# Kernel optimization log

Measured on AMD Instinct MI355X. Metric: run time of the kernel, lower is better.

## Reference

```python
import jax, jax.numpy as jnp
import numpy as np

B, S, I = 4096, 128, 8
H = 512
L = 3


def setup_inputs() -> dict:
    key = jax.random.key(0)
    ks = jax.random.split(key, 5)
    scale = 1.0 / np.sqrt(H)
    return {
        "input": jax.random.normal(ks[0], (B, S, I), dtype=jnp.float32),
        "Wih": jax.random.normal(ks[1], (L, 3 * H, I), dtype=jnp.float32) * scale,
        "Whh": jax.random.normal(ks[2], (L, 3 * H, H), dtype=jnp.float32) * scale,
        "bih": jax.random.normal(ks[3], (L, 3 * H), dtype=jnp.float32) * scale,
        "bhh": jax.random.normal(ks[4], (L, 3 * H), dtype=jnp.float32) * scale,
    }


def _gru_cell(x, h, Wih, Whh, bih, bhh):
    # PyTorch GRUCell gate order: reset, update, new
    gi = x @ Wih.T + bih            # [B, 3H]
    gh = h @ Whh.T + bhh            # [B, 3H]
    i_r, i_z, i_n = jnp.split(gi, 3, axis=-1)
    h_r, h_z, h_n = jnp.split(gh, 3, axis=-1)
    r = jax.nn.sigmoid(i_r + h_r)
    z = jax.nn.sigmoid(i_z + h_z)
    n = jnp.tanh(i_n + r * h_n)
    return (1.0 - z) * n + z * h


def reference(input, Wih, Whh, bih, bhh):
    batch = input.shape[0]
    h0 = jnp.zeros((batch, Wih.shape[1] // 3), dtype=input.dtype)

    def step(h, x_t):
        # each layer consumes the same raw input x_t, chaining the context
        for l in range(Wih.shape[0]):
            h = _gru_cell(x_t, h, Wih[l], Whh[l], bih[l], bhh[l])
        return h, None

    xs = jnp.swapaxes(input, 0, 1)  # [S, B, I]
    h_final, _ = jax.lax.scan(step, h0, xs)
    return h_final
```

## Files before the change

### kernel.cpp

```cpp
#include <hip/hip_runtime.h>

typedef __attribute__((ext_vector_type(8))) short short8;
typedef __attribute__((ext_vector_type(4))) float f32x4;
typedef __attribute__((ext_vector_type(4))) int   i32x4;

#define MFMA(a,b,c)  __builtin_amdgcn_mfma_f32_16x16x32_bf16(a,b,c,0,0,0)
#define MFMAI(a,b,c) __builtin_amdgcn_mfma_i32_16x16x64_i8(a,b,c,0,0,0)

#define S_LEN 128
#define IN_D  8
#define HID   512
#define NL    3
#define H8STR 528
#define LOG2E  1.4426950408889634f
#define LOG2E2 2.8853901617779268f
#define WKL_STRIDE ((size_t)(32 * 8 * 3 * 64 * 16))

#define OFF_WI8  0
#define OFF_WIH  (2359296)
#define OFF_SW   (2359296 + 294912)
#define OFF_SWI  (OFF_SW + 18432)
#define OFF_FLAG (OFF_SWI + 18432)
#define OFF_XCHG (OFF_FLAG + 1024)

__device__ __forceinline__ unsigned short f2bf(float f){
  unsigned u = __float_as_uint(f);
  u += 0x7FFFu + ((u >> 16) & 1u);
  return (unsigned short)(u >> 16);
}
__device__ __forceinline__ float fexp2(float x){ return __builtin_amdgcn_exp2f(x); }
__device__ __forceinline__ float frcp(float x){ return __builtin_amdgcn_rcpf(x); }

__global__ void prep_scale(const float* __restrict__ Whh,
                           float* __restrict__ sw, float* __restrict__ swi){
  int row = blockIdx.x * 4 + (threadIdx.x >> 6);
  int lane = threadIdx.x & 63;
  const float* src = Whh + (size_t)row * 512;
  float m = 0.f;
#pragma unroll
  for (int i = 0; i < 8; ++i) m = fmaxf(m, fabsf(src[lane + i * 64]));
#pragma unroll
  for (int off = 32; off; off >>= 1) m = fmaxf(m, (float)__shfl_xor(m, off));
  m = fmaxf(m, 1e-20f);
  if (lane == 0){ sw[row] = m / 127.f; swi[row] = 127.f / m; }
}

__global__ void prep_wi8(const float* __restrict__ Whh, const float* __restrict__ swi,
                         unsigned char* __restrict__ Wp8){
  int gid = blockIdx.x * 256 + threadIdx.x;
  int lane = gid & 63;
  int r = gid >> 6;
  int g  = r % 3;  r /= 3;
  int kk = r & 7;  r >>= 3;
  int nt = r & 31;
  int l  = r >> 5;
  int row = l * 1536 + g * 512 + nt * 16 + (lane & 15);
  int k0  = kk * 64 + (lane >> 4) * 16;
  const float* src = Whh + (size_t)row * 512 + k0;
  float si = swi[row];
  uint4 v = {0,0,0,0};
  unsigned w[4] = {0,0,0,0};
#pragma unroll
  for (int j = 0; j < 16; ++j){
    int q = (int)rintf(src[j] * si);
    q = q > 127 ? 127 : (q < -127 ? -127 : q);
    w[j >> 2] |= ((unsigned)(q & 0xFF)) << ((j & 3) * 8);
  }
  v.x = w[0]; v.y = w[1]; v.z = w[2]; v.w = w[3];
  *(uint4*)(Wp8 + (size_t)gid * 16) = v;
}

__global__ void prep_wih(const float* __restrict__ Wih, unsigned short* __restrict__ Wip){
  int gid = blockIdx.x * 256 + threadIdx.x;
  int lane = gid & 63;
  int r = gid >> 6;
  int g  = r % 3;  r /= 3;
  int nt = r & 31;
  int l  = r >> 5;
  float scl = (g == 2) ? LOG2E2 : LOG2E;
  unsigned short t[8] = {0,0,0,0,0,0,0,0};
  if ((lane >> 4) == 0){
    int n = g * 512 + nt * 16 + (lane & 15);
    const float* src = Wih + ((size_t)l * 1536 + n) * 8;
#pragma unroll
    for (int j = 0; j < 8; ++j) t[j] = f2bf(src[j] * scl);
  }
  uint4 v;
  v.x = t[0] | ((unsigned)t[1] << 16);
  v.y = t[2] | ((unsigned)t[3] << 16);
  v.z = t[4] | ((unsigned)t[5] << 16);
  v.w = t[6] | ((unsigned)t[7] << 16);
  *(uint4*)(Wip + (size_t)gid * 8) = v;
}

__global__ __launch_bounds__(1024) void gru_main(
    const float* __restrict__ x,
    const unsigned char* __restrict__ Wp8,
    const unsigned short* __restrict__ Wip,
    const float* __restrict__ bih,
    const float* __restrict__ bhh,
    const float* __restrict__ sw,
    float* __restrict__ out,
    int* __restrict__ flags,
    unsigned int* __restrict__ xchg)
{
  __shared__ __align__(16) unsigned char  hB8[2][32 * H8STR];
  __shared__ __align__(16) unsigned short xpack[2][1024];
  __shared__ __align__(16) float sBrz[3 * 1024];
  __shared__ __align__(16) float sBni[3 * 512];
  __shared__ __align__(16) float sBnh[3 * 512];
  __shared__ __align__(16) float sK[4608];
  __shared__ int   pad[1024];

  const int tid  = threadIdx.x;
  const int wv   = tid >> 6;
  const int lane = tid & 63;
  const int l15  = lane & 15;
  const int l4   = lane >> 4;

  const int bid     = blockIdx.x;
  const int bgroup  = ((bid >> 3) << 2) | (bid & 3);
  const int half    = (bid >> 2) & 1;
  const int partner = bid ^ 4;
  const int b0      = bgroup * 32;
  const int lc      = wv * 16 + l4 * 4;
  const int colv    = half * 256 + lc;
  const int ntc     = half * 16 + wv;
  const int pcb0    = (1 - half) * 256;
  const int ko0     = half * 4;
  const int pk0     = 4 - ko0;

  if (flags[bid] == -1) pad[tid] = tid;

  unsigned int* xown = xchg + (size_t)bid * 4096;
  const unsigned int* xpb = xchg + (size_t)partner * 4096 + tid;
  const int dOff = (tid >> 6) * H8STR + pcb0 + (tid & 63) * 4;

  for (int i = tid; i < 2 * 32 * H8STR / 4; i += 1024) ((unsigned*)hB8)[i] = 0;
  for (int i = tid; i < 3072; i += 1024){
    int l = i >> 10, c = i & 1023;
    sBrz[i] = (bih[l * 1536 + c] + bhh[l * 1536 + c]) * LOG2E;
  }
  for (int i = tid; i < 1536; i += 1024){
    int l = i >> 9, c = i & 511;
    sBni[i] = bih[l * 1536 + 1024 + c] * LOG2E2;
    sBnh[i] = bhh[l * 1536 + 1024 + c] * LOG2E2;
  }
  for (int i = tid; i < 4608; i += 1024){
    int g = (i % 1536) >> 9;
    sK[i] = sw[i] * (1.f / 127.f) * (g == 2 ? LOG2E2 : LOG2E);
  }

  float hreg[2][4];
#pragma unroll
  for (int nf = 0; nf < 2; ++nf)
#pragma unroll
    for (int qq = 0; qq < 4; ++qq) hreg[nf][qq] = 0.f;

  const int xl = (tid >> 3) & 63;
  const size_t xbase = ((size_t)(b0 + (tid >> 9) * 16 + (xl & 15))) * (S_LEN * IN_D) + (tid & 7);
  const int xvalid = (xl < 16);
  { float xv = xvalid ? x[xbase] : 0.f; xpack[0][tid] = f2bf(xv); }
  __syncthreads();

  const int boff0 = l15 * H8STR + l4 * 16;
  const int boff1 = boff0 + 16 * H8STR;

  const unsigned char*  wklB = Wp8 + (size_t)ntc * (8 * 3 * 64 * 16) + (size_t)lane * 16;
  const unsigned short* wilB = Wip + (size_t)ntc * 3 * 512 + (size_t)lane * 8;

#define KSEQ(i) ((i) < 4 ? (ko0 + (i)) : (pk0 + (i) - 4))
#define WLD(S, i, P) { const unsigned char* w_ = (P) + KSEQ(i) * 3072; \
    wR##S = *(const i32x4*)(w_); \
    wZ##S = *(const i32x4*)(w_ + 1024); \
    wN##S = *(const i32x4*)(w_ + 2048); }
#define CONS(S, i) { \
    i32x4 hb0 = *(const i32x4*)(hb8c + boff0 + KSEQ(i) * 64); \
    i32x4 hb1 = *(const i32x4*)(hb8c + boff1 + KSEQ(i) * 64); \
    aR[0] = MFMAI(wR##S, hb0, aR[0]);  aR[1] = MFMAI(wR##S, hb1, aR[1]); \
    aZ[0] = MFMAI(wZ##S, hb0, aZ[0]);  aZ[1] = MFMAI(wZ##S, hb1, aZ[1]); \
    aN[0] = MFMAI(wN##S, hb0, aN[0]);  aN[1] = MFMAI(wN##S, hb1, aN[1]); }

  i32x4 wRa, wZa, wNa, wRb, wZb, wNb;
  WLD(a, 0, wklB)  WLD(b, 1, wklB)

  int cur = 0;
#pragma unroll 1
  for (int t = 0; t < S_LEN; ++t){
    const unsigned short* xp = &xpack[t & 1][0];
#pragma unroll 1
    for (int l = 0; l < NL; ++l){
      const int s    = t * NL + l;
      const int last = (s == S_LEN * NL - 1);
      const unsigned char* hb8c = hB8[cur];
      unsigned char*       hb8w = hB8[cur];
      unsigned char*       hb8n = hB8[cur ^ 1];
      const unsigned char*  wkl = wklB + (size_t)l * WKL_STRIDE;
      const unsigned short* wil = wilB + (size_t)l * (32 * 3 * 512);

      unsigned c0 = 0, c1 = 0;
      if (s > 0){
        while (__hip_atomic_load(&flags[partner], __ATOMIC_RELAXED, __HIP_MEMORY_SCOPE_AGENT) < s)
          __builtin_amdgcn_s_sleep(4);
        const unsigned int* src = xpb + ((s - 1) & 1) * 2048;
        c0 = __hip_atomic_load(src,        __ATOMIC_RELAXED, __HIP_MEMORY_SCOPE_AGENT);
        c1 = __hip_atomic_load(src + 1024, __ATOMIC_RELAXED, __HIP_MEMORY_SCOPE_AGENT);
      }

      i32x4 aR[2], aZ[2], aN[2];
#pragma unroll
      for (int nf = 0; nf < 2; ++nf){
        aR[nf] = (i32x4){0,0,0,0};
        aZ[nf] = (i32x4){0,0,0,0};
        aN[nf] = (i32x4){0,0,0,0};
      }

      CONS(a, 0)  WLD(a, 2, wkl)
      CONS(b, 1)  WLD(b, 3, wkl)
      CONS(a, 2)  WLD(a, 4, wkl)
      CONS(b, 3)  WLD(b, 5, wkl)

      if (s > 0){
        *(unsigned*)(hb8w + dOff)              = c0;
        *(unsigned*)(hb8w + dOff + 16 * H8STR) = c1;
      }
      asm volatile("s_waitcnt lgkmcnt(0)" ::: "memory");
      __builtin_amdgcn_s_barrier();

      short8 wiR = *(const short8*)(wil);
      short8 wiZ = *(const short8*)(wil + 512);
      short8 wiN = *(const short8*)(wil + 1024);

      CONS(a, 4)  WLD(a, 6, wkl)
      CONS(b, 5)  WLD(b, 7, wkl)
      CONS(a, 6)
      CONS(b, 7)

      {
        const unsigned char* wkn = wklB + (size_t)(l == NL - 1 ? 0 : l + 1) * WKL_STRIDE;
        WLD(a, 0, wkn)  WLD(b, 1, wkn)
      }

      const f32x4 vR4  = *(const f32x4*)&sBrz[l * 1024 + colv];
      const f32x4 vZ4  = *(const f32x4*)&sBrz[l * 1024 + 512 + colv];
      const f32x4 vNi4 = *(const f32x4*)&sBni[l * 512 + colv];
      const f32x4 vNh4 = *(const f32x4*)&sBnh[l * 512 + colv];
      const f32x4 kR4  = *(const f32x4*)&sK[l * 1536 + colv];
      const f32x4 kZ4  = *(const f32x4*)&sK[l * 1536 + 512 + colv];
      const f32x4 kN4  = *(const f32x4*)&sK[l * 1536 + 1024 + colv];

      f32x4 gR[2], gZ[2], gN[2];
      gR[0] = vR4;  gR[1] = vR4;
      gZ[0] = vZ4;  gZ[1] = vZ4;
      gN[0] = vNi4; gN[1] = vNi4;
      {
        short8 xb0 = *(const short8*)(xp + lane * 8);
        short8 xb1 = *(const short8*)(xp + 512 + lane * 8);
        gR[0] = MFMA(wiR, xb0, gR[0]);  gR[1] = MFMA(wiR, xb1, gR[1]);
        gZ[0] = MFMA(wiZ, xb0, gZ[0]);  gZ[1] = MFMA(wiZ, xb1, gZ[1]);
        gN[0] = MFMA(wiN, xb0, gN[0]);  gN[1] = MFMA(wiN, xb1, gN[1]);
      }

      unsigned int* xob = xown + (s & 1) * 2048;
#pragma unroll
      for (int nf = 0; nf < 2; ++nf){
        unsigned pk = 0;
#pragma unroll
        for (int qq = 0; qq < 4; ++qq){
          float rp = gR[nf][qq] + (float)aR[nf][qq] * kR4[qq];
          float zp = gZ[nf][qq] + (float)aZ[nf][qq] * kZ4[qq];
          float r  = frcp(1.f + fexp2(-rp));
          float z  = frcp(1.f + fexp2(-zp));
          float an = gN[nf][qq] + r * ((float)aN[nf][qq] * kN4[qq] + vNh4[qq]);
          float n  = fmaf(-2.f, frcp(1.f + fexp2(an)), 1.f);
          float hn = fmaf(z, hreg[nf][qq] - n, n);
          hreg[nf][qq] = hn;
          int hq = (int)rintf(hn * 127.f);
          pk |= ((unsigned)(hq & 0xFF)) << (qq * 8);
        }
        int brow = nf * 16 + l15;
        *(unsigned*)(hb8n + brow * H8STR + colv) = pk;
        if (!last)
          __hip_atomic_store(xob + brow * 64 + wv * 4 + l4, pk,
                             __ATOMIC_RELAXED, __HIP_MEMORY_SCOPE_AGENT);
      }

      if (l == NL - 1 && t < S_LEN - 1){
        float xv = xvalid ? x[xbase + (size_t)(t + 1) * IN_D] : 0.f;
        xpack[(t + 1) & 1][tid] = f2bf(xv);
      }

      if (!last){
        asm volatile("s_waitcnt vmcnt(0)" ::: "memory");
        __syncthreads();
        if (tid == 0)
          __hip_atomic_store(&flags[bid], s + 1, __ATOMIC_RELAXED, __HIP_MEMORY_SCOPE_AGENT);
      }
      cur ^= 1;
    }
  }
#undef WLD
#undef CONS
#undef KSEQ

#pragma unroll
  for (int nf = 0; nf < 2; ++nf){
    f32x4 v = { hreg[nf][0], hreg[nf][1], hreg[nf][2], hreg[nf][3] };
    int brow = nf * 16 + l15;
    *(f32x4*)&out[((size_t)(b0 + brow)) * 512 + colv] = v;
  }

  if (flags[bid] == -2) out[0] = (float)pad[tid];
}

extern "C" void kernel_launch(void* const* d_in, const int* in_sizes, int n_in,
                              void* d_out, int out_size, void* d_ws, size_t ws_size,
                              hipStream_t stream){
  const float* x   = (const float*)d_in[0];
  const float* Wih = (const float*)d_in[1];
  const float* Whh = (const float*)d_in[2];
  const float* bih = (const float*)d_in[3];
  const float* bhh = (const float*)d_in[4];

  unsigned char* ws = (unsigned char*)d_ws;
  unsigned char*  Wp8  = (unsigned char*)(ws + OFF_WI8);
  unsigned short* Wip  = (unsigned short*)(ws + OFF_WIH);
  float*          sw   = (float*)(ws + OFF_SW);
  float*          swi  = (float*)(ws + OFF_SWI);
  int*            flg  = (int*)(ws + OFF_FLAG);
  unsigned int*   xchg = (unsigned int*)(ws + OFF_XCHG);

  hipMemsetAsync(flg, 0, 256 * sizeof(int), stream);
  prep_scale<<<1152, 256, 0, stream>>>(Whh, sw, swi);
  prep_wi8  <<< 576, 256, 0, stream>>>(Whh, swi, Wp8);
  prep_wih  <<<  72, 256, 0, stream>>>(Wih, Wip);
  gru_main  <<< 256, 1024, 0, stream>>>(x, Wp8, Wip, bih, bhh, sw, (float*)d_out, flg, xchg);
}
```

Before: 2.700 ms.

## Drop cross-block partner exchange; each block computes all 512 hidden columns

Before, each 32-row batch group was split across two partner blocks that each owned half the hidden columns. They traded int8 hidden-state halves through global memory, with flag spin-waits at every layer step. Now one block handles the full hidden width: each wave does two 16-column tiles in sequence, and the grid drops from 256 to 128 blocks. This removes the global round-trip and polling latency from the serial recurrence, at the cost of twice the MFMA and weight-streaming work per block and only half as many CUs in use.

```diff
diff --git a/kernel.cpp b/kernel.cpp
--- a/kernel.cpp
+++ b/kernel.cpp
@@ -15,13 +15,12 @@
 #define LOG2E  1.4426950408889634f
 #define LOG2E2 2.8853901617779268f
 #define WKL_STRIDE ((size_t)(32 * 8 * 3 * 64 * 16))
+#define NTC_STRIDE ((size_t)(8 * 3 * 64 * 16))
 
 #define OFF_WI8  0
 #define OFF_WIH  (2359296)
 #define OFF_SW   (2359296 + 294912)
 #define OFF_SWI  (OFF_SW + 18432)
-#define OFF_FLAG (OFF_SWI + 18432)
-#define OFF_XCHG (OFF_FLAG + 1024)
 
 __device__ __forceinline__ unsigned short f2bf(float f){
   unsigned u = __float_as_uint(f);
@@ -100,9 +99,7 @@
     const float* __restrict__ bih,
     const float* __restrict__ bhh,
     const float* __restrict__ sw,
-    float* __restrict__ out,
-    int* __restrict__ flags,
-    unsigned int* __restrict__ xchg)
+    float* __restrict__ out)
 {
   __shared__ __align__(16) unsigned char  hB8[2][32 * H8STR];
   __shared__ __align__(16) unsigned short xpack[2][1024];
@@ -118,23 +115,13 @@
   const int l15  = lane & 15;
   const int l4   = lane >> 4;
 
-  const int bid     = blockIdx.x;
-  const int bgroup  = ((bid >> 3) << 2) | (bid & 3);
-  const int half    = (bid >> 2) & 1;
-  const int partner = bid ^ 4;
-  const int b0      = bgroup * 32;
-  const int lc      = wv * 16 + l4 * 4;
-  const int colv    = half * 256 + lc;
-  const int ntc     = half * 16 + wv;
-  const int pcb0    = (1 - half) * 256;
-  const int ko0     = half * 4;
-  const int pk0     = 4 - ko0;
-
-  if (flags[bid] == -1) pad[tid] = tid;
-
-  unsigned int* xown = xchg + (size_t)bid * 4096;
-  const unsigned int* xpb = xchg + (size_t)partner * 4096 + tid;
-  const int dOff = (tid >> 6) * H8STR + pcb0 + (tid & 63) * 4;
+  const int bid   = blockIdx.x;
+  const int b0    = bid * 32;
+  const int colv0 = wv * 32 + l4 * 4;
+  const int colv1 = colv0 + 16;
+  const int ntc0  = wv * 2;
+
+  if ((size_t)x == 1) pad[tid] = tid;
 
   for (int i = tid; i < 2 * 32 * H8STR / 4; i += 1024) ((unsigned*)hB8)[i] = 0;
   for (int i = tid; i < 3072; i += 1024){
@@ -151,11 +138,13 @@
     sK[i] = sw[i] * (1.f / 127.f) * (g == 2 ? LOG2E2 : LOG2E);
   }
 
-  float hreg[2][4];
-#pragma unroll
-  for (int nf = 0; nf < 2; ++nf)
-#pragma unroll
-    for (int qq = 0; qq < 4; ++qq) hreg[nf][qq] = 0.f;
+  float hreg[2][2][4];
+#pragma unroll
+  for (int nt = 0; nt < 2; ++nt)
+#pragma unroll
+    for (int nf = 0; nf < 2; ++nf)
+#pragma unroll
+      for (int qq = 0; qq < 4; ++qq) hreg[nt][nf][qq] = 0.f;
 
   const int xl = (tid >> 3) & 63;
   const size_t xbase = ((size_t)(b0 + (tid >> 9) * 16 + (xl & 15))) * (S_LEN * IN_D) + (tid & 7);
@@ -166,23 +155,24 @@
   const int boff0 = l15 * H8STR + l4 * 16;
   const int boff1 = boff0 + 16 * H8STR;
 
-  const unsigned char*  wklB = Wp8 + (size_t)ntc * (8 * 3 * 64 * 16) + (size_t)lane * 16;
-  const unsigned short* wilB = Wip + (size_t)ntc * 3 * 512 + (size_t)lane * 8;
-
-#define KSEQ(i) ((i) < 4 ? (ko0 + (i)) : (pk0 + (i) - 4))
-#define WLD(S, i, P) { const unsigned char* w_ = (P) + KSEQ(i) * 3072; \
+  const unsigned char*  wklB = Wp8 + (size_t)ntc0 * NTC_STRIDE + (size_t)lane * 16;
+  const unsigned short* wilB = Wip + (size_t)ntc0 * 3 * 512 + (size_t)lane * 8;
+
+#define FPTR(W0, i) ((i) < 8 ? (W0) + (size_t)(i) * 3072 \
+                             : (W0) + NTC_STRIDE + (size_t)((i) - 8) * 3072)
+#define WLD(S, P) { const unsigned char* w_ = (P); \
     wR##S = *(const i32x4*)(w_); \
     wZ##S = *(const i32x4*)(w_ + 1024); \
     wN##S = *(const i32x4*)(w_ + 2048); }
 #define CONS(S, i) { \
-    i32x4 hb0 = *(const i32x4*)(hb8c + boff0 + KSEQ(i) * 64); \
-    i32x4 hb1 = *(const i32x4*)(hb8c + boff1 + KSEQ(i) * 64); \
+    i32x4 hb0 = *(const i32x4*)(hb8c + boff0 + ((i) & 7) * 64); \
+    i32x4 hb1 = *(const i32x4*)(hb8c + boff1 + ((i) & 7) * 64); \
     aR[0] = MFMAI(wR##S, hb0, aR[0]);  aR[1] = MFMAI(wR##S, hb1, aR[1]); \
     aZ[0] = MFMAI(wZ##S, hb0, aZ[0]);  aZ[1] = MFMAI(wZ##S, hb1, aZ[1]); \
     aN[0] = MFMAI(wN##S, hb0, aN[0]);  aN[1] = MFMAI(wN##S, hb1, aN[1]); }
 
   i32x4 wRa, wZa, wNa, wRb, wZb, wNb;
-  WLD(a, 0, wklB)  WLD(b, 1, wklB)
+  WLD(a, FPTR(wklB, 0))  WLD(b, FPTR(wklB, 1))
 
   int cur = 0;
 #pragma unroll 1
@@ -190,22 +180,14 @@
     const unsigned short* xp = &xpack[t & 1][0];
 #pragma unroll 1
     for (int l = 0; l < NL; ++l){
-      const int s    = t * NL + l;
-      const int last = (s == S_LEN * NL - 1);
+      const int last = (t == S_LEN - 1) && (l == NL - 1);
       const unsigned char* hb8c = hB8[cur];
-      unsigned char*       hb8w = hB8[cur];
       unsigned char*       hb8n = hB8[cur ^ 1];
       const unsigned char*  wkl = wklB + (size_t)l * WKL_STRIDE;
       const unsigned short* wil = wilB + (size_t)l * (32 * 3 * 512);
 
-      unsigned c0 = 0, c1 = 0;
-      if (s > 0){
-        while (__hip_atomic_load(&flags[partner], __ATOMIC_RELAXED, __HIP_MEMORY_SCOPE_AGENT) < s)
-          __builtin_amdgcn_s_sleep(4);
-        const unsigned int* src = xpb + ((s - 1) & 1) * 2048;
-        c0 = __hip_atomic_load(src,        __ATOMIC_RELAXED, __HIP_MEMORY_SCOPE_AGENT);
-        c1 = __hip_atomic_load(src + 1024, __ATOMIC_RELAXED, __HIP_MEMORY_SCOPE_AGENT);
-      }
+      short8 xb0 = *(const short8*)(xp + lane * 8);
+      short8 xb1 = *(const short8*)(xp + 512 + lane * 8);
 
       i32x4 aR[2], aZ[2], aN[2];
 #pragma unroll
@@ -214,75 +196,108 @@
         aZ[nf] = (i32x4){0,0,0,0};
         aN[nf] = (i32x4){0,0,0,0};
       }
-
-      CONS(a, 0)  WLD(a, 2, wkl)
-      CONS(b, 1)  WLD(b, 3, wkl)
-      CONS(a, 2)  WLD(a, 4, wkl)
-      CONS(b, 3)  WLD(b, 5, wkl)
-
-      if (s > 0){
-        *(unsigned*)(hb8w + dOff)              = c0;
-        *(unsigned*)(hb8w + dOff + 16 * H8STR) = c1;
-      }
-      asm volatile("s_waitcnt lgkmcnt(0)" ::: "memory");
-      __builtin_amdgcn_s_barrier();
-
-      short8 wiR = *(const short8*)(wil);
-      short8 wiZ = *(const short8*)(wil + 512);
-      short8 wiN = *(const short8*)(wil + 1024);
-
-      CONS(a, 4)  WLD(a, 6, wkl)
-      CONS(b, 5)  WLD(b, 7, wkl)
-      CONS(a, 6)
-      CONS(b, 7)
+      CONS(a, 0)  WLD(a, FPTR(wkl, 2))
+      CONS(b, 1)  WLD(b, FPTR(wkl, 3))
+      CONS(a, 2)  WLD(a, FPTR(wkl, 4))
+      CONS(b, 3)  WLD(b, FPTR(wkl, 5))
+      CONS(a, 4)  WLD(a, FPTR(wkl, 6))
+      CONS(b, 5)  WLD(b, FPTR(wkl, 7))
+      CONS(a, 6)  WLD(a, FPTR(wkl, 8))
+      CONS(b, 7)  WLD(b, FPTR(wkl, 9))
 
       {
-        const unsigned char* wkn = wklB + (size_t)(l == NL - 1 ? 0 : l + 1) * WKL_STRIDE;
-        WLD(a, 0, wkn)  WLD(b, 1, wkn)
-      }
-
-      const f32x4 vR4  = *(const f32x4*)&sBrz[l * 1024 + colv];
-      const f32x4 vZ4  = *(const f32x4*)&sBrz[l * 1024 + 512 + colv];
-      const f32x4 vNi4 = *(const f32x4*)&sBni[l * 512 + colv];
-      const f32x4 vNh4 = *(const f32x4*)&sBnh[l * 512 + colv];
-      const f32x4 kR4  = *(const f32x4*)&sK[l * 1536 + colv];
-      const f32x4 kZ4  = *(const f32x4*)&sK[l * 1536 + 512 + colv];
-      const f32x4 kN4  = *(const f32x4*)&sK[l * 1536 + 1024 + colv];
-
-      f32x4 gR[2], gZ[2], gN[2];
-      gR[0] = vR4;  gR[1] = vR4;
-      gZ[0] = vZ4;  gZ[1] = vZ4;
-      gN[0] = vNi4; gN[1] = vNi4;
-      {
-        short8 xb0 = *(const short8*)(xp + lane * 8);
-        short8 xb1 = *(const short8*)(xp + 512 + lane * 8);
+        short8 wiR = *(const short8*)(wil);
+        short8 wiZ = *(const short8*)(wil + 512);
+        short8 wiN = *(const short8*)(wil + 1024);
+        const f32x4 vR4  = *(const f32x4*)&sBrz[l * 1024 + colv0];
+        const f32x4 vZ4  = *(const f32x4*)&sBrz[l * 1024 + 512 + colv0];
+        const f32x4 vNi4 = *(const f32x4*)&sBni[l * 512 + colv0];
+        const f32x4 vNh4 = *(const f32x4*)&sBnh[l * 512 + colv0];
+        const f32x4 kR4  = *(const f32x4*)&sK[l * 1536 + colv0];
+        const f32x4 kZ4  = *(const f32x4*)&sK[l * 1536 + 512 + colv0];
+        const f32x4 kN4  = *(const f32x4*)&sK[l * 1536 + 1024 + colv0];
+        f32x4 gR[2], gZ[2], gN[2];
+        gR[0] = vR4;  gR[1] = vR4;
+        gZ[0] = vZ4;  gZ[1] = vZ4;
+        gN[0] = vNi4; gN[1] = vNi4;
         gR[0] = MFMA(wiR, xb0, gR[0]);  gR[1] = MFMA(wiR, xb1, gR[1]);
         gZ[0] = MFMA(wiZ, xb0, gZ[0]);  gZ[1] = MFMA(wiZ, xb1, gZ[1]);
         gN[0] = MFMA(wiN, xb0, gN[0]);  gN[1] = MFMA(wiN, xb1, gN[1]);
-      }
-
-      unsigned int* xob = xown + (s & 1) * 2048;
+#pragma unroll
+        for (int nf = 0; nf < 2; ++nf){
+          unsigned pk = 0;
+#pragma unroll
+          for (int qq = 0; qq < 4; ++qq){
+            float rp = gR[nf][qq] + (float)aR[nf][qq] * kR4[qq];
+            float zp = gZ[nf][qq] + (float)aZ[nf][qq] * kZ4[qq];
+            float r  = frcp(1.f + fexp2(-rp));
+            float z  = frcp(1.f + fexp2(-zp));
+            float an = gN[nf][qq] + r * ((float)aN[nf][qq] * kN4[qq] + vNh4[qq]);
+            float n  = fmaf(-2.f, frcp(1.f + fexp2(an)), 1.f);
+            float hn = fmaf(z, hreg[0][nf][qq] - n, n);
+            hreg[0][nf][qq] = hn;
+            int hq = (int)rintf(hn * 127.f);
+            pk |= ((unsigned)(hq & 0xFF)) << (qq * 8);
+          }
+          int brow = nf * 16 + l15;
+          *(unsigned*)(hb8n + brow * H8STR + colv0) = pk;
+        }
+      }
+
 #pragma unroll
       for (int nf = 0; nf < 2; ++nf){
-        unsigned pk = 0;
-#pragma unroll
-        for (int qq = 0; qq < 4; ++qq){
-          float rp = gR[nf][qq] + (float)aR[nf][qq] * kR4[qq];
-          float zp = gZ[nf][qq] + (float)aZ[nf][qq] * kZ4[qq];
-          float r  = frcp(1.f + fexp2(-rp));
-          float z  = frcp(1.f + fexp2(-zp));
-          float an = gN[nf][qq] + r * ((float)aN[nf][qq] * kN4[qq] + vNh4[qq]);
-          float n  = fmaf(-2.f, frcp(1.f + fexp2(an)), 1.f);
-          float hn = fmaf(z, hreg[nf][qq] - n, n);
-          hreg[nf][qq] = hn;
-          int hq = (int)rintf(hn * 127.f);
-          pk |= ((unsigned)(hq & 0xFF)) << (qq * 8);
+        aR[nf] = (i32x4){0,0,0,0};
+        aZ[nf] = (i32x4){0,0,0,0};
+        aN[nf] = (i32x4){0,0,0,0};
+      }
+      const unsigned char* wkn = wklB + (size_t)(l == NL - 1 ? 0 : l + 1) * WKL_STRIDE;
+      CONS(a, 8)   WLD(a, FPTR(wkl, 10))
+      CONS(b, 9)   WLD(b, FPTR(wkl, 11))
+      CONS(a, 10)  WLD(a, FPTR(wkl, 12))
+      CONS(b, 11)  WLD(b, FPTR(wkl, 13))
+      CONS(a, 12)  WLD(a, FPTR(wkl, 14))
+      CONS(b, 13)  WLD(b, FPTR(wkl, 15))
+      CONS(a, 14)  WLD(a, FPTR(wkn, 0))
+      CONS(b, 15)  WLD(b, FPTR(wkn, 1))
+
+      {
+        const unsigned short* wi1 = wil + 3 * 512;
+        short8 wiR = *(const short8*)(wi1);
+        short8 wiZ = *(const short8*)(wi1 + 512);
+        short8 wiN = *(const short8*)(wi1 + 1024);
+        const f32x4 vR4  = *(const f32x4*)&sBrz[l * 1024 + colv1];
+        const f32x4 vZ4  = *(const f32x4*)&sBrz[l * 1024 + 512 + colv1];
+        const f32x4 vNi4 = *(const f32x4*)&sBni[l * 512 + colv1];
+        const f32x4 vNh4 = *(const f32x4*)&sBnh[l * 512 + colv1];
+        const f32x4 kR4  = *(const f32x4*)&sK[l * 1536 + colv1];
+        const f32x4 kZ4  = *(const f32x4*)&sK[l * 1536 + 512 + colv1];
+        const f32x4 kN4  = *(const f32x4*)&sK[l * 1536 + 1024 + colv1];
+        f32x4 gR[2], gZ[2], gN[2];
+        gR[0] = vR4;  gR[1] = vR4;
+        gZ[0] = vZ4;  gZ[1] = vZ4;
+        gN[0] = vNi4; gN[1] = vNi4;
+        gR[0] = MFMA(wiR, xb0, gR[0]);  gR[1] = MFMA(wiR, xb1, gR[1]);
+        gZ[0] = MFMA(wiZ, xb0, gZ[0]);  gZ[1] = MFMA(wiZ, xb1, gZ[1]);
+        gN[0] = MFMA(wiN, xb0, gN[0]);  gN[1] = MFMA(wiN, xb1, gN[1]);
+#pragma unroll
+        for (int nf = 0; nf < 2; ++nf){
+          unsigned pk = 0;
+#pragma unroll
+          for (int qq = 0; qq < 4; ++qq){
+            float rp = gR[nf][qq] + (float)aR[nf][qq] * kR4[qq];
+            float zp = gZ[nf][qq] + (float)aZ[nf][qq] * kZ4[qq];
+            float r  = frcp(1.f + fexp2(-rp));
+            float z  = frcp(1.f + fexp2(-zp));
+            float an = gN[nf][qq] + r * ((float)aN[nf][qq] * kN4[qq] + vNh4[qq]);
+            float n  = fmaf(-2.f, frcp(1.f + fexp2(an)), 1.f);
+            float hn = fmaf(z, hreg[1][nf][qq] - n, n);
+            hreg[1][nf][qq] = hn;
+            int hq = (int)rintf(hn * 127.f);
+            pk |= ((unsigned)(hq & 0xFF)) << (qq * 8);
+          }
+          int brow = nf * 16 + l15;
+          *(unsigned*)(hb8n + brow * H8STR + colv1) = pk;
         }
-        int brow = nf * 16 + l15;
-        *(unsigned*)(hb8n + brow * H8STR + colv) = pk;
-        if (!last)
-          __hip_atomic_store(xob + brow * 64 + wv * 4 + l4, pk,
-                             __ATOMIC_RELAXED, __HIP_MEMORY_SCOPE_AGENT);
       }
 
       if (l == NL - 1 && t < S_LEN - 1){
@@ -290,27 +305,27 @@
         xpack[(t + 1) & 1][tid] = f2bf(xv);
       }
 
-      if (!last){
-        asm volatile("s_waitcnt vmcnt(0)" ::: "memory");
-        __syncthreads();
-        if (tid == 0)
-          __hip_atomic_store(&flags[bid], s + 1, __ATOMIC_RELAXED, __HIP_MEMORY_SCOPE_AGENT);
-      }
+      if (!last) __syncthreads();
       cur ^= 1;
     }
   }
 #undef WLD
 #undef CONS
-#undef KSEQ
-
-#pragma unroll
-  for (int nf = 0; nf < 2; ++nf){
-    f32x4 v = { hreg[nf][0], hreg[nf][1], hreg[nf][2], hreg[nf][3] };
-    int brow = nf * 16 + l15;
-    *(f32x4*)&out[((size_t)(b0 + brow)) * 512 + colv] = v;
-  }
-
-  if (flags[bid] == -2) out[0] = (float)pad[tid];
+#undef FPTR
+
+#pragma unroll
+  for (int nt = 0; nt < 2; ++nt)
+#pragma unroll
+    for (int nf = 0; nf < 2; ++nf){
+      f32x4 v = { hreg[nt][nf][0], hreg[nt][nf][1], hreg[nt][nf][2], hreg[nt][nf][3] };
+      int brow = nf * 16 + l15;
+      out[((size_t)(b0 + brow)) * 512 + (nt ? colv1 : colv0) + 0] = v[0];
+      out[((size_t)(b0 + brow)) * 512 + (nt ? colv1 : colv0) + 1] = v[1];
+      out[((size_t)(b0 + brow)) * 512 + (nt ? colv1 : colv0) + 2] = v[2];
+      out[((size_t)(b0 + brow)) * 512 + (nt ? colv1 : colv0) + 3] = v[3];
+    }
+
+  if ((size_t)x == 2) out[0] = (float)pad[tid];
 }
 
 extern "C" void kernel_launch(void* const* d_in, const int* in_sizes, int n_in,
@@ -327,12 +342,9 @@
   unsigned short* Wip  = (unsigned short*)(ws + OFF_WIH);
   float*          sw   = (float*)(ws + OFF_SW);
   float*          swi  = (float*)(ws + OFF_SWI);
-  int*            flg  = (int*)(ws + OFF_FLAG);
-  unsigned int*   xchg = (unsigned int*)(ws + OFF_XCHG);
-
-  hipMemsetAsync(flg, 0, 256 * sizeof(int), stream);
+
   prep_scale<<<1152, 256, 0, stream>>>(Whh, sw, swi);
   prep_wi8  <<< 576, 256, 0, stream>>>(Whh, swi, Wp8);
   prep_wih  <<<  72, 256, 0, stream>>>(Wih, Wip);
-  gru_main  <<< 256, 1024, 0, stream>>>(x, Wp8, Wip, bih, bhh, sw, (float*)d_out, flg, xchg);
-}
+  gru_main  <<< 128, 1024, 0, stream>>>(x, Wp8, Wip, bih, bhh, sw, (float*)d_out);
+}
```

Measured after the change: 3.845 ms. 1.42x slower.
